# Optimization experiments

Measured on AMD Instinct MI355X. Metric: run time of the kernel, lower is better.

## Reference

```python
import jax, jax.numpy as jnp
import numpy as np

N, E, D, H = 50000, 1600000, 256, 256
EPS = 1e-5

def prelu(x, a):
    return jnp.where(x >= 0, x, a * x)

def batch_norm(x, gamma, beta):
    # training-mode BatchNorm1d: stats over the node (batch) dim
    mu = jnp.mean(x, axis=0)
    var = jnp.var(x, axis=0)
    return (x - mu) * jax.lax.rsqrt(var + EPS) * gamma + beta

def gcn_conv(x, edge_index, W, b):
    # PyG GCNConv: h = XW, add self-loops, symmetric norm, scatter-add, + bias
    h = x @ W
    n = x.shape[0]
    row = jnp.concatenate([edge_index[0], jnp.arange(n)])
    col = jnp.concatenate([edge_index[1], jnp.arange(n)])
    w = jnp.ones(row.shape[0], dtype=x.dtype)
    deg = jax.ops.segment_sum(w, col, num_segments=n)
    dinv = jnp.where(deg > 0, jax.lax.rsqrt(deg), 0.0)
    norm = dinv[row] * w * dinv[col]  # [E+N]
    msg = h[row] * norm[:, None]      # [E+N, H] gathered messages
    out = jax.ops.segment_sum(msg, col, num_segments=n)
    return out + b

def setup_inputs() -> dict:
    key = jax.random.key(0)
    ks = jax.random.split(key, 10)
    x = jax.random.normal(ks[0], (N, D), dtype=jnp.float32)
    edge_index = jax.random.randint(ks[1], (2, E), 0, N).astype(jnp.int64)
    s1 = 1.0 / np.sqrt(D)
    s2 = 1.0 / np.sqrt(H)
    return {
        "x": x,
        "edge_index": edge_index,
        "W1": jax.random.uniform(ks[2], (D, H), jnp.float32, -s1, s1),
        "b1": jnp.zeros((H,), jnp.float32),
        "W2": jax.random.uniform(ks[3], (H, H), jnp.float32, -s2, s2),
        "b2": jnp.zeros((H,), jnp.float32),
        "prelu_a": jnp.asarray(0.25, jnp.float32),
        "bn_gamma": jnp.ones((H,), jnp.float32),
        "bn_beta": jnp.zeros((H,), jnp.float32),
        "proj_W": jax.random.uniform(ks[4], (H, H), jnp.float32, -s2, s2),
        "proj_b": jnp.zeros((H,), jnp.float32),
        "pbn_gamma": jnp.ones((H,), jnp.float32),
        "pbn_beta": jnp.zeros((H,), jnp.float32),
        "prelu2_a": jnp.asarray(0.25, jnp.float32),
    }

def reference(x, edge_index, W1, b1, W2, b2, prelu_a, bn_gamma, bn_beta,
              proj_W, proj_b, pbn_gamma, pbn_beta, prelu2_a):
    # eval-mode dropout (identity); BN uses batch stats
    z = prelu(gcn_conv(x, edge_index, W1, b1), prelu_a)
    z = prelu(gcn_conv(z, edge_index, W2, b2), prelu_a)
    z = batch_norm(z, bn_gamma, bn_beta)
    p = prelu(batch_norm(z @ proj_W + proj_b, pbn_gamma, pbn_beta), prelu2_a)
    return (z, p)
```

## Files before the change

### kernel.cpp

```cpp
#include <hip/hip_runtime.h>
#include <hip/hip_bf16.h>


#define CAP 96
#define NPB 128
#define CHUNK 4096
#define SEGBIG 4608
#define MAXBKT 512

typedef __attribute__((ext_vector_type(8))) short short8;
typedef __attribute__((ext_vector_type(4))) float f32x4;

__device__ __forceinline__ float bf2f(unsigned short u) {
    union { unsigned int i; float f; } v; v.i = ((unsigned int)u) << 16; return v.f;
}
__device__ __forceinline__ unsigned short f2bf(float f) {
    __hip_bfloat16 h = __float2bfloat16(f);
    return *reinterpret_cast<unsigned short*>(&h);
}

__global__ __launch_bounds__(256) void k_zero(int* segcnt, int nbkt, float* stats, float* dinv, int N) {
    int i = blockIdx.x * 256 + threadIdx.x;
    if (i < nbkt) segcnt[i] = 0;
    if (i < 2048) stats[i] = 0.0f;
    if (i == 0) dinv[N] = 0.0f;
}

__global__ __launch_bounds__(256) void k_binh(const int* __restrict__ row, const int* __restrict__ col,
                                              unsigned* __restrict__ bins, int* __restrict__ segcnt,
                                              int E, int nbkt) {
    __shared__ int hist[MAXBKT];
    __shared__ int base[MAXBKT];
    int e0 = blockIdx.x * CHUNK;
    int eend = e0 + CHUNK; if (eend > E) eend = E;
    for (int b = threadIdx.x; b < nbkt; b += 256) hist[b] = 0;
    __syncthreads();
    for (int e = e0 + threadIdx.x; e < eend; e += 256)
        atomicAdd(&hist[col[e] >> 7], 1);
    __syncthreads();
    for (int b = threadIdx.x; b < nbkt; b += 256) {
        int h = hist[b];
        base[b] = h ? atomicAdd(&segcnt[b], h) : 0;
        hist[b] = 0;
    }
    __syncthreads();
    for (int e = e0 + threadIdx.x; e < eend; e += 256) {
        int v = col[e], r = row[e];
        int b = v >> 7;
        int p = base[b] + atomicAdd(&hist[b], 1);
        if (p < SEGBIG) bins[(size_t)b * SEGBIG + p] = ((unsigned)r << 7) | (unsigned)(v & (NPB - 1));
    }
}

__global__ __launch_bounds__(256) void k_csr(const unsigned* __restrict__ bins, const int* __restrict__ segcnt,
                                             int* __restrict__ csr, int* __restrict__ fillp,
                                             float* __restrict__ dinv, int N) {
    __shared__ int cnt[NPB];
    int bkt = blockIdx.x;
    if (threadIdx.x < NPB) cnt[threadIdx.x] = 0;
    __syncthreads();
    int m = segcnt[bkt]; if (m > SEGBIG) m = SEGBIG;
    const unsigned* b = bins + (size_t)bkt * SEGBIG;
    for (int i = threadIdx.x; i < m; i += 256) {
        unsigned ent = b[i];
        int loc = (int)(ent & (NPB - 1));
        int r   = (int)(ent >> 7);
        int p = atomicAdd(&cnt[loc], 1);
        if (p < CAP) csr[(size_t)(bkt * NPB + loc) * CAP + p] = r;
    }
    __syncthreads();
    if (threadIdx.x < NPB) {
        int v = bkt * NPB + threadIdx.x;
        if (v < N) {
            int c = cnt[threadIdx.x];
            int real = c < CAP ? c : CAP;
            int pc = (real + 7) & ~7;
            if (pc > CAP) pc = CAP;
            int* lst = csr + (size_t)v * CAP;
            for (int p = real; p < pc; ++p) lst[p] = N;
            fillp[v] = pc;
            dinv[v] = rsqrtf(1.0f + (float)c);
        }
    }
}

__global__ __launch_bounds__(256) void k_castx(const float* __restrict__ x, unsigned short* __restrict__ xb, size_t n4) {
    size_t stride = (size_t)gridDim.x * blockDim.x;
    for (size_t i = (size_t)blockIdx.x * blockDim.x + threadIdx.x; i < n4; i += stride) {
        float4 v = ((const float4*)x)[i];
        ushort4 o; o.x = f2bf(v.x); o.y = f2bf(v.y); o.z = f2bf(v.z); o.w = f2bf(v.w);
        ((ushort4*)xb)[i] = o;
    }
}

__global__ __launch_bounds__(256) void k_wt(const float* __restrict__ W, unsigned short* __restrict__ Wt) {
    __shared__ float t[32][33];
    int bx = blockIdx.x * 32, by = blockIdx.y * 32;
    int x = threadIdx.x & 31, y = threadIdx.x >> 5;
#pragma unroll
    for (int i = 0; i < 32; i += 8)
        t[y + i][x] = W[(size_t)(by + y + i) * 256 + bx + x];
    __syncthreads();
#pragma unroll
    for (int i = 0; i < 32; i += 8)
        Wt[(size_t)(bx + y + i) * 256 + by + x] = f2bf(t[x][y + i]);
}

__global__ __launch_bounds__(256) void k_gemm_bf16(const unsigned short* __restrict__ A,
                                                   const unsigned short* __restrict__ Bt,
                                                   unsigned short* __restrict__ C, int M) {
    __shared__ unsigned short As[128 * 64];
    __shared__ unsigned short Bs[128 * 64];
    int tid  = threadIdx.x;
    int lane = tid & 63, wid = tid >> 6;
    int wr = wid >> 1, wc = wid & 1;
    int row0 = blockIdx.x * 128;
    int col0 = blockIdx.y * 128;

    f32x4 acc[4][4];
#pragma unroll
    for (int m = 0; m < 4; ++m)
#pragma unroll
        for (int n = 0; n < 4; ++n) acc[m][n] = f32x4{0.f, 0.f, 0.f, 0.f};

    int srow = lane >> 3;
    int sk   = (lane & 7) * 8;

    for (int k0 = 0; k0 < 256; k0 += 64) {
#pragma unroll
        for (int i = 0; i < 4; ++i) {
            int u = i * 4 + wid;
            int arow = row0 + u * 8 + srow;
            if (arow >= M) arow = M - 1;
            const unsigned short* ga = A  + (size_t)arow * 256 + k0 + sk;
            const unsigned short* gb = Bt + (size_t)(col0 + u * 8 + srow) * 256 + k0 + sk;
            __builtin_amdgcn_global_load_lds((const __attribute__((address_space(1))) void*)ga,
                (__attribute__((address_space(3))) void*)(As + u * 512), 16, 0, 0);
            __builtin_amdgcn_global_load_lds((const __attribute__((address_space(1))) void*)gb,
                (__attribute__((address_space(3))) void*)(Bs + u * 512), 16, 0, 0);
        }
        __syncthreads();
#pragma unroll
        for (int kk = 0; kk < 64; kk += 32) {
            short8 a[4], b[4];
#pragma unroll
            for (int m = 0; m < 4; ++m)
                a[m] = *(const short8*)(As + (wr * 64 + m * 16 + (lane & 15)) * 64 + kk + (lane >> 4) * 8);
#pragma unroll
            for (int n = 0; n < 4; ++n)
                b[n] = *(const short8*)(Bs + (wc * 64 + n * 16 + (lane & 15)) * 64 + kk + (lane >> 4) * 8);
#pragma unroll
            for (int m = 0; m < 4; ++m)
#pragma unroll
                for (int n = 0; n < 4; ++n)
                    acc[m][n] = __builtin_amdgcn_mfma_f32_16x16x32_bf16(a[m], b[n], acc[m][n], 0, 0, 0);
        }
        __syncthreads();
    }

    int crow = row0 + wr * 64;
    int ccol = col0 + wc * 64;
#pragma unroll
    for (int m = 0; m < 4; ++m)
#pragma unroll
        for (int r = 0; r < 4; ++r) {
            int rr = crow + m * 16 + (lane >> 4) * 4 + r;
            if (rr < M) {
#pragma unroll
                for (int n = 0; n < 4; ++n)
                    C[(size_t)rr * 256 + ccol + n * 16 + (lane & 15)] = f2bf(acc[m][n][r]);
            }
        }
}

__global__ __launch_bounds__(256) void k_agg_bf(const unsigned short* __restrict__ h,
                                                unsigned short* __restrict__ outb,
                                                const float* __restrict__ dinv, const int* __restrict__ csr,
                                                const int* __restrict__ fillp, const float* __restrict__ bias,
                                                const float* __restrict__ aptr, int N) {
    int wv = threadIdx.x >> 6, lane = threadIdx.x & 63;
    int v = blockIdx.x * 4 + wv;
    if (v >= N) return;
    const ushort4* h4 = (const ushort4*)h;
    float dv = dinv[v];
    ushort4 hv = h4[(size_t)v * 64 + lane];
    float s0 = dv * bf2f(hv.x), s1 = dv * bf2f(hv.y), s2 = dv * bf2f(hv.z), s3 = dv * bf2f(hv.w);
    int n = fillp[v];
    const int* lst = csr + (size_t)v * CAP;
    for (int i = 0; i < n; i += 8) {
        int u0 = lst[i],     u1 = lst[i + 1], u2 = lst[i + 2], u3 = lst[i + 3];
        int u4 = lst[i + 4], u5 = lst[i + 5], u6 = lst[i + 6], u7 = lst[i + 7];
        ushort4 a0 = h4[(size_t)u0 * 64 + lane];
        ushort4 a1 = h4[(size_t)u1 * 64 + lane];
        ushort4 a2 = h4[(size_t)u2 * 64 + lane];
        ushort4 a3 = h4[(size_t)u3 * 64 + lane];
        ushort4 a4 = h4[(size_t)u4 * 64 + lane];
        ushort4 a5 = h4[(size_t)u5 * 64 + lane];
        ushort4 a6 = h4[(size_t)u6 * 64 + lane];
        ushort4 a7 = h4[(size_t)u7 * 64 + lane];
        float d0 = dinv[u0], d1 = dinv[u1], d2 = dinv[u2], d3 = dinv[u3];
        float d4 = dinv[u4], d5 = dinv[u5], d6 = dinv[u6], d7 = dinv[u7];
        s0 += d0 * bf2f(a0.x) + d1 * bf2f(a1.x) + d2 * bf2f(a2.x) + d3 * bf2f(a3.x)
            + d4 * bf2f(a4.x) + d5 * bf2f(a5.x) + d6 * bf2f(a6.x) + d7 * bf2f(a7.x);
        s1 += d0 * bf2f(a0.y) + d1 * bf2f(a1.y) + d2 * bf2f(a2.y) + d3 * bf2f(a3.y)
            + d4 * bf2f(a4.y) + d5 * bf2f(a5.y) + d6 * bf2f(a6.y) + d7 * bf2f(a7.y);
        s2 += d0 * bf2f(a0.z) + d1 * bf2f(a1.z) + d2 * bf2f(a2.z) + d3 * bf2f(a3.z)
            + d4 * bf2f(a4.z) + d5 * bf2f(a5.z) + d6 * bf2f(a6.z) + d7 * bf2f(a7.z);
        s3 += d0 * bf2f(a0.w) + d1 * bf2f(a1.w) + d2 * bf2f(a2.w) + d3 * bf2f(a3.w)
            + d4 * bf2f(a4.w) + d5 * bf2f(a5.w) + d6 * bf2f(a6.w) + d7 * bf2f(a7.w);
    }
    float a = *aptr;
    float4 bb = *(const float4*)(bias + lane * 4);
    float o0 = dv * s0 + bb.x, o1 = dv * s1 + bb.y, o2 = dv * s2 + bb.z, o3 = dv * s3 + bb.w;
    o0 = o0 >= 0.f ? o0 : a * o0;
    o1 = o1 >= 0.f ? o1 : a * o1;
    o2 = o2 >= 0.f ? o2 : a * o2;
    o3 = o3 >= 0.f ? o3 : a * o3;
    ushort4 o; o.x = f2bf(o0); o.y = f2bf(o1); o.z = f2bf(o2); o.w = f2bf(o3);
    ((ushort4*)outb)[(size_t)v * 64 + lane] = o;
}

__global__ __launch_bounds__(256) void k_bnstats_v(const unsigned short* __restrict__ X, float* __restrict__ sums, int N) {
    int w = threadIdx.x >> 6, lane = threadIdx.x & 63;
    int c4 = lane * 4;
    float4 s = {0.f, 0.f, 0.f, 0.f}, q = {0.f, 0.f, 0.f, 0.f};
    int rstride = gridDim.x * 4;
    for (int r = blockIdx.x * 4 + w; r < N; r += rstride) {
        ushort4 x4 = ((const ushort4*)X)[(size_t)r * 64 + lane];
        float a = bf2f(x4.x), b = bf2f(x4.y), c = bf2f(x4.z), d = bf2f(x4.w);
        s.x += a; s.y += b; s.z += c; s.w += d;
        q.x += a * a; q.y += b * b; q.z += c * c; q.w += d * d;
    }
    atomicAdd(&sums[c4 + 0], s.x); atomicAdd(&sums[c4 + 1], s.y);
    atomicAdd(&sums[c4 + 2], s.z); atomicAdd(&sums[c4 + 3], s.w);
    atomicAdd(&sums[256 + c4 + 0], q.x); atomicAdd(&sums[256 + c4 + 1], q.y);
    atomicAdd(&sums[256 + c4 + 2], q.z); atomicAdd(&sums[256 + c4 + 3], q.w);
}

__global__ __launch_bounds__(256) void k_bnfinal(float* stats, const float* __restrict__ gamma,
                                                 const float* __restrict__ beta, float invN) {
    int c = threadIdx.x;
    float mu = stats[c] * invN;
    float var = stats[256 + c] * invN - mu * mu;
    float rstd = rsqrtf(var + 1e-5f);
    float sc = rstd * gamma[c];
    stats[512 + c] = sc;
    stats[768 + c] = beta[c] - mu * sc;
}

__global__ __launch_bounds__(256) void k_bnapply_z(const unsigned short* __restrict__ in,
                                                   float* __restrict__ zout, unsigned short* __restrict__ zb,
                                                   const float* __restrict__ scale, const float* __restrict__ shift,
                                                   size_t n4) {
    size_t stride = (size_t)gridDim.x * blockDim.x;
    for (size_t i = (size_t)blockIdx.x * blockDim.x + threadIdx.x; i < n4; i += stride) {
        int c4 = (int)(i & 63) * 4;
        ushort4 x4 = ((const ushort4*)in)[i];
        float4 sc = *(const float4*)(scale + c4);
        float4 sh = *(const float4*)(shift + c4);
        float4 y;
        y.x = bf2f(x4.x) * sc.x + sh.x;
        y.y = bf2f(x4.y) * sc.y + sh.y;
        y.z = bf2f(x4.z) * sc.z + sh.z;
        y.w = bf2f(x4.w) * sc.w + sh.w;
        ((float4*)zout)[i] = y;
        ushort4 o; o.x = f2bf(y.x); o.y = f2bf(y.y); o.z = f2bf(y.z); o.w = f2bf(y.w);
        ((ushort4*)zb)[i] = o;
    }
}

__global__ __launch_bounds__(256) void k_bnapply_p(const unsigned short* __restrict__ in,
                                                   float* __restrict__ pout,
                                                   const float* __restrict__ scale, const float* __restrict__ shift,
                                                   const float* __restrict__ aptr, size_t n4) {
    size_t stride = (size_t)gridDim.x * blockDim.x;
    float a = *aptr;
    for (size_t i = (size_t)blockIdx.x * blockDim.x + threadIdx.x; i < n4; i += stride) {
        int c4 = (int)(i & 63) * 4;
        ushort4 x4 = ((const ushort4*)in)[i];
        float4 sc = *(const float4*)(scale + c4);
        float4 sh = *(const float4*)(shift + c4);
        float4 y;
        y.x = bf2f(x4.x) * sc.x + sh.x;
        y.y = bf2f(x4.y) * sc.y + sh.y;
        y.z = bf2f(x4.z) * sc.z + sh.z;
        y.w = bf2f(x4.w) * sc.w + sh.w;
        y.x = y.x >= 0.f ? y.x : a * y.x;
        y.y = y.y >= 0.f ? y.y : a * y.y;
        y.z = y.z >= 0.f ? y.z : a * y.z;
        y.w = y.w >= 0.f ? y.w : a * y.w;
        ((float4*)pout)[i] = y;
    }
}

extern "C" void kernel_launch(void* const* d_in, const int* in_sizes, int n_in,
                              void* d_out, int out_size, void* d_ws, size_t ws_size,
                              hipStream_t stream) {
    const float* x     = (const float*)d_in[0];
    const int*   ei    = (const int*)d_in[1];
    const float* W1    = (const float*)d_in[2];
    const float* b1    = (const float*)d_in[3];
    const float* W2    = (const float*)d_in[4];
    const float* b2    = (const float*)d_in[5];
    const float* aptr  = (const float*)d_in[6];
    const float* gamma = (const float*)d_in[7];
    const float* beta  = (const float*)d_in[8];
    const float* projW = (const float*)d_in[9];
    const float* pgamma = (const float*)d_in[11];
    const float* pbeta  = (const float*)d_in[12];
    const float* a2ptr  = (const float*)d_in[13];

    int N = in_sizes[0] / 256;
    int E = in_sizes[1] / 2;
    const int* row = ei;
    const int* col = ei + E;

    float* out  = (float*)d_out;
    float* zout = out;
    float* pout = out + (size_t)N * 256;

    int nbkt = (N + NPB - 1) / NPB;

    unsigned short* B0 = (unsigned short*)d_ws;
    unsigned short* B1 = B0 + (size_t)N * 256;
    unsigned short* B2 = B1 + (size_t)N * 256;
    unsigned short* Wt = B2 + (size_t)N * 256;
    float* dinv  = (float*)(Wt + 3 * 65536);
    int*   fillp = (int*)(dinv + N + 1);
    int*   csr   = fillp + N;
    float* stats = (float*)(csr + (size_t)N * CAP);
    int*   segcnt= (int*)(stats + 2048);
    unsigned* bins = (unsigned*)(segcnt + MAXBKT);

    int nb_binh = (E + CHUNK - 1) / CHUNK;
    dim3 ggrid((N + 127) / 128, 2);
    dim3 wgrid(8, 8);
    int  agrid = (N + 3) / 4;
    size_t n4 = (size_t)N * 64;

    k_zero <<<(2048 + 255) / 256, 256, 0, stream>>>(segcnt, nbkt, stats, dinv, N);
    k_binh <<<nb_binh, 256, 0, stream>>>(row, col, bins, segcnt, E, nbkt);
    k_csr  <<<nbkt, 256, 0, stream>>>(bins, segcnt, csr, fillp, dinv, N);
    k_castx<<<2048, 256, 0, stream>>>(x, B0, n4);
    k_wt   <<<wgrid, 256, 0, stream>>>(W1,    Wt);
    k_wt   <<<wgrid, 256, 0, stream>>>(W2,    Wt + 65536);
    k_wt   <<<wgrid, 256, 0, stream>>>(projW, Wt + 131072);

    k_gemm_bf16<<<ggrid, 256, 0, stream>>>(B0, Wt, B1, N);
    k_agg_bf   <<<agrid, 256, 0, stream>>>(B1, B2, dinv, csr, fillp, b1, aptr, N);
    k_gemm_bf16<<<ggrid, 256, 0, stream>>>(B2, Wt + 65536, B1, N);
    k_agg_bf   <<<agrid, 256, 0, stream>>>(B1, B0, dinv, csr, fillp, b2, aptr, N);
    k_bnstats_v<<<128, 256, 0, stream>>>(B0, stats, N);
    k_bnfinal  <<<1, 256, 0, stream>>>(stats, gamma, beta, 1.0f / (float)N);
    k_bnapply_z<<<2048, 256, 0, stream>>>(B0, zout, B2, stats + 512, stats + 768, n4);
    k_gemm_bf16<<<ggrid, 256, 0, stream>>>(B2, Wt + 131072, B1, N);
    k_bnstats_v<<<128, 256, 0, stream>>>(B1, stats + 1024, N);
    k_bnfinal  <<<1, 256, 0, stream>>>(stats + 1024, pgamma, pbeta, 1.0f / (float)N);
    k_bnapply_p<<<2048, 256, 0, stream>>>(B1, pout, stats + 1536, stats + 1792, a2ptr, n4);
}
```

Baseline: 682.4 us.

## Prescale GEMM output by source dinv and drop per-edge dinv gathers in aggregation

The GEMM epilogue now stages the tile through LDS and writes coalesced 16-byte rows, optionally multiplying each row by dinv[row] so the aggregation reads pre-normalised features. The aggregation loop then skips the per-neighbour dinv gather and multiply, adds an explicit zero padding row at index N for the padded sentinel entries, and unrolls 16 neighbours per iteration with padding to multiples of 16. This cuts scattered loads in the edge loop and improves GEMM store coalescing. The cost is an extra bf16 rounding after scaling, more padding entries to load, and an LDS staging pass in the epilogue.

```diff
diff --git a/kernel.cpp b/kernel.cpp
--- a/kernel.cpp
+++ b/kernel.cpp
@@ -24,6 +24,10 @@
     if (i < nbkt) segcnt[i] = 0;
     if (i < 2048) stats[i] = 0.0f;
     if (i == 0) dinv[N] = 0.0f;
+}
+
+__global__ __launch_bounds__(256) void k_zrow(unsigned short* hs, int N) {
+    ((ushort4*)hs)[(size_t)N * 64 + threadIdx.x % 64] = ushort4{0, 0, 0, 0};
 }
 
 __global__ __launch_bounds__(256) void k_binh(const int* __restrict__ row, const int* __restrict__ col,
@@ -74,7 +78,7 @@
         if (v < N) {
             int c = cnt[threadIdx.x];
             int real = c < CAP ? c : CAP;
-            int pc = (real + 7) & ~7;
+            int pc = (real + 15) & ~15;
             if (pc > CAP) pc = CAP;
             int* lst = csr + (size_t)v * CAP;
             for (int p = real; p < pc; ++p) lst[p] = N;
@@ -108,9 +112,12 @@
 
 __global__ __launch_bounds__(256) void k_gemm_bf16(const unsigned short* __restrict__ A,
                                                    const unsigned short* __restrict__ Bt,
-                                                   unsigned short* __restrict__ C, int M) {
-    __shared__ unsigned short As[128 * 64];
-    __shared__ unsigned short Bs[128 * 64];
+                                                   unsigned short* __restrict__ C,
+                                                   const float* __restrict__ dinv,
+                                                   int use_scale, int M) {
+    __shared__ unsigned short buf[16384];
+    unsigned short* As = buf;
+    unsigned short* Bs = buf + 8192;
     int tid  = threadIdx.x;
     int lane = tid & 63, wid = tid >> 6;
     int wr = wid >> 1, wc = wid & 1;
@@ -158,22 +165,37 @@
         __syncthreads();
     }
 
-    int crow = row0 + wr * 64;
-    int ccol = col0 + wc * 64;
 #pragma unroll
     for (int m = 0; m < 4; ++m)
 #pragma unroll
         for (int r = 0; r < 4; ++r) {
-            int rr = crow + m * 16 + (lane >> 4) * 4 + r;
-            if (rr < M) {
-#pragma unroll
-                for (int n = 0; n < 4; ++n)
-                    C[(size_t)rr * 256 + ccol + n * 16 + (lane & 15)] = f2bf(acc[m][n][r]);
+            int lr = wr * 64 + m * 16 + (lane >> 4) * 4 + r;
+#pragma unroll
+            for (int n = 0; n < 4; ++n)
+                buf[lr * 128 + wc * 64 + n * 16 + (lane & 15)] = f2bf(acc[m][n][r]);
+        }
+    __syncthreads();
+#pragma unroll
+    for (int j = 0; j < 8; ++j) {
+        int c = j * 256 + tid;
+        int r = c >> 4, cc = c & 15;
+        int grow = row0 + r;
+        if (grow < M) {
+            short8 v = *(const short8*)(buf + r * 128 + cc * 8);
+            if (use_scale) {
+                float d = dinv[grow];
+                short8 o;
+#pragma unroll
+                for (int t = 0; t < 8; ++t)
+                    o[t] = (short)f2bf(bf2f((unsigned short)v[t]) * d);
+                v = o;
             }
-        }
-}
-
-__global__ __launch_bounds__(256) void k_agg_bf(const unsigned short* __restrict__ h,
+            *(short8*)(C + (size_t)grow * 256 + col0 + cc * 8) = v;
+        }
+    }
+}
+
+__global__ __launch_bounds__(256) void k_agg_bf(const unsigned short* __restrict__ hs,
                                                 unsigned short* __restrict__ outb,
                                                 const float* __restrict__ dinv, const int* __restrict__ csr,
                                                 const int* __restrict__ fillp, const float* __restrict__ bias,
@@ -181,41 +203,32 @@
     int wv = threadIdx.x >> 6, lane = threadIdx.x & 63;
     int v = blockIdx.x * 4 + wv;
     if (v >= N) return;
-    const ushort4* h4 = (const ushort4*)h;
+    const ushort4* h4 = (const ushort4*)hs;
     float dv = dinv[v];
     ushort4 hv = h4[(size_t)v * 64 + lane];
-    float s0 = dv * bf2f(hv.x), s1 = dv * bf2f(hv.y), s2 = dv * bf2f(hv.z), s3 = dv * bf2f(hv.w);
+    float s0 = bf2f(hv.x), s1 = bf2f(hv.y), s2 = bf2f(hv.z), s3 = bf2f(hv.w);
     int n = fillp[v];
     const int* lst = csr + (size_t)v * CAP;
-    for (int i = 0; i < n; i += 8) {
-        int u0 = lst[i],     u1 = lst[i + 1], u2 = lst[i + 2], u3 = lst[i + 3];
-        int u4 = lst[i + 4], u5 = lst[i + 5], u6 = lst[i + 6], u7 = lst[i + 7];
-        ushort4 a0 = h4[(size_t)u0 * 64 + lane];
-        ushort4 a1 = h4[(size_t)u1 * 64 + lane];
-        ushort4 a2 = h4[(size_t)u2 * 64 + lane];
-        ushort4 a3 = h4[(size_t)u3 * 64 + lane];
-        ushort4 a4 = h4[(size_t)u4 * 64 + lane];
-        ushort4 a5 = h4[(size_t)u5 * 64 + lane];
-        ushort4 a6 = h4[(size_t)u6 * 64 + lane];
-        ushort4 a7 = h4[(size_t)u7 * 64 + lane];
-        float d0 = dinv[u0], d1 = dinv[u1], d2 = dinv[u2], d3 = dinv[u3];
-        float d4 = dinv[u4], d5 = dinv[u5], d6 = dinv[u6], d7 = dinv[u7];
-        s0 += d0 * bf2f(a0.x) + d1 * bf2f(a1.x) + d2 * bf2f(a2.x) + d3 * bf2f(a3.x)
-            + d4 * bf2f(a4.x) + d5 * bf2f(a5.x) + d6 * bf2f(a6.x) + d7 * bf2f(a7.x);
-        s1 += d0 * bf2f(a0.y) + d1 * bf2f(a1.y) + d2 * bf2f(a2.y) + d3 * bf2f(a3.y)
-            + d4 * bf2f(a4.y) + d5 * bf2f(a5.y) + d6 * bf2f(a6.y) + d7 * bf2f(a7.y);
-        s2 += d0 * bf2f(a0.z) + d1 * bf2f(a1.z) + d2 * bf2f(a2.z) + d3 * bf2f(a3.z)
-            + d4 * bf2f(a4.z) + d5 * bf2f(a5.z) + d6 * bf2f(a6.z) + d7 * bf2f(a7.z);
-        s3 += d0 * bf2f(a0.w) + d1 * bf2f(a1.w) + d2 * bf2f(a2.w) + d3 * bf2f(a3.w)
-            + d4 * bf2f(a4.w) + d5 * bf2f(a5.w) + d6 * bf2f(a6.w) + d7 * bf2f(a7.w);
-    }
-    float a = *aptr;
+    for (int i = 0; i < n; i += 16) {
+        int u[16];
+        ushort4 a[16];
+#pragma unroll
+        for (int t = 0; t < 16; ++t) u[t] = lst[i + t];
+#pragma unroll
+        for (int t = 0; t < 16; ++t) a[t] = h4[(size_t)u[t] * 64 + lane];
+#pragma unroll
+        for (int t = 0; t < 16; ++t) {
+            s0 += bf2f(a[t].x); s1 += bf2f(a[t].y);
+            s2 += bf2f(a[t].z); s3 += bf2f(a[t].w);
+        }
+    }
+    float al = *aptr;
     float4 bb = *(const float4*)(bias + lane * 4);
     float o0 = dv * s0 + bb.x, o1 = dv * s1 + bb.y, o2 = dv * s2 + bb.z, o3 = dv * s3 + bb.w;
-    o0 = o0 >= 0.f ? o0 : a * o0;
-    o1 = o1 >= 0.f ? o1 : a * o1;
-    o2 = o2 >= 0.f ? o2 : a * o2;
-    o3 = o3 >= 0.f ? o3 : a * o3;
+    o0 = o0 >= 0.f ? o0 : al * o0;
+    o1 = o1 >= 0.f ? o1 : al * o1;
+    o2 = o2 >= 0.f ? o2 : al * o2;
+    o3 = o3 >= 0.f ? o3 : al * o3;
     ushort4 o; o.x = f2bf(o0); o.y = f2bf(o1); o.z = f2bf(o2); o.w = f2bf(o3);
     ((ushort4*)outb)[(size_t)v * 64 + lane] = o;
 }
@@ -321,10 +334,11 @@
 
     int nbkt = (N + NPB - 1) / NPB;
 
+    size_t rowsz = (size_t)(N + 1) * 256;
     unsigned short* B0 = (unsigned short*)d_ws;
-    unsigned short* B1 = B0 + (size_t)N * 256;
-    unsigned short* B2 = B1 + (size_t)N * 256;
-    unsigned short* Wt = B2 + (size_t)N * 256;
+    unsigned short* B1 = B0 + rowsz;
+    unsigned short* B2 = B1 + rowsz;
+    unsigned short* Wt = B2 + rowsz;
     float* dinv  = (float*)(Wt + 3 * 65536);
     int*   fillp = (int*)(dinv + N + 1);
     int*   csr   = fillp + N;
@@ -338,7 +352,8 @@
     int  agrid = (N + 3) / 4;
     size_t n4 = (size_t)N * 64;
 
-    k_zero <<<(2048 + 255) / 256, 256, 0, stream>>>(segcnt, nbkt, stats, dinv, N);
+    k_zero <<<8, 256, 0, stream>>>(segcnt, nbkt, stats, dinv, N);
+    k_zrow <<<1, 64, 0, stream>>>(B1, N);
     k_binh <<<nb_binh, 256, 0, stream>>>(row, col, bins, segcnt, E, nbkt);
     k_csr  <<<nbkt, 256, 0, stream>>>(bins, segcnt, csr, fillp, dinv, N);
     k_castx<<<2048, 256, 0, stream>>>(x, B0, n4);
@@ -346,14 +361,15 @@
     k_wt   <<<wgrid, 256, 0, stream>>>(W2,    Wt + 65536);
     k_wt   <<<wgrid, 256, 0, stream>>>(projW, Wt + 131072);
 
-    k_gemm_bf16<<<ggrid, 256, 0, stream>>>(B0, Wt, B1, N);
+    k_gemm_bf16<<<ggrid, 256, 0, stream>>>(B0, Wt, B1, dinv, 1, N);
     k_agg_bf   <<<agrid, 256, 0, stream>>>(B1, B2, dinv, csr, fillp, b1, aptr, N);
-    k_gemm_bf16<<<ggrid, 256, 0, stream>>>(B2, Wt + 65536, B1, N);
+    k_zrow <<<1, 64, 0, stream>>>(B1, N);
+    k_gemm_bf16<<<ggrid, 256, 0, stream>>>(B2, Wt + 65536, B1, dinv, 1, N);
     k_agg_bf   <<<agrid, 256, 0, stream>>>(B1, B0, dinv, csr, fillp, b2, aptr, N);
     k_bnstats_v<<<128, 256, 0, stream>>>(B0, stats, N);
     k_bnfinal  <<<1, 256, 0, stream>>>(stats, gamma, beta, 1.0f / (float)N);
     k_bnapply_z<<<2048, 256, 0, stream>>>(B0, zout, B2, stats + 512, stats + 768, n4);
-    k_gemm_bf16<<<ggrid, 256, 0, stream>>>(B2, Wt + 131072, B1, N);
+    k_gemm_bf16<<<ggrid, 256, 0, stream>>>(B2, Wt + 131072, B1, dinv, 0, N);
     k_bnstats_v<<<128, 256, 0, stream>>>(B1, stats + 1024, N);
     k_bnfinal  <<<1, 256, 0, stream>>>(stats + 1024, pgamma, pbeta, 1.0f / (float)N);
     k_bnapply_p<<<2048, 256, 0, stream>>>(B1, pout, stats + 1536, stats + 1792, a2ptr, n4);
```

Measured after the change: 677.3 us. Within noise of the previous version (-0.7%).
